# Kernel optimization log

Hardware: AMD Instinct MI355X
Metric: run time of the kernel (lower is better)

Reference implementation:

```python
import jax, jax.numpy as jnp
import numpy as np

B, L = 512, 260          # batch, raw input length
N_EMB, E_DIM = 8192, 128 * 65
NC = 16                   # num_classes


def setup_inputs() -> dict:
    key = jax.random.key(0)
    ks = jax.random.split(key, 12)
    rn = lambda k, shp, s: jax.random.normal(k, shp, jnp.float32) * s
    return {
        "x": rn(ks[0], (B, L), 1.0),
        # VQ codebook, init uniform(-1/K, 1/K) as in reference VQ-VAE
        "codebook": jax.random.uniform(ks[1], (N_EMB, E_DIM), jnp.float32, -1.0 / N_EMB, 1.0 / N_EMB),
        # encoder: Conv1d(1,64,k4,s2,p1) -> ReLU -> Conv1d(64,128,k4,s2,p1)
        "conv1_w": rn(ks[2], (64, 1, 4), 0.3), "conv1_b": jnp.zeros((64,), jnp.float32),
        "conv2_w": rn(ks[3], (128, 64, 4), 0.06), "conv2_b": jnp.zeros((128,), jnp.float32),
        # decoder: ConvT1d(128,64,k4,s2,p1) -> ReLU -> ConvT1d(64,1,k4,s2,p1); torch weight layout (in,out,k)
        "dec1_w": rn(ks[4], (128, 64, 4), 0.04), "dec1_b": jnp.zeros((64,), jnp.float32),
        "dec2_w": rn(ks[5], (64, 1, 4), 0.06), "dec2_b": jnp.zeros((1,), jnp.float32),
        # multitask head: Linear(4160, NC); torch layout (out,in)
        "mt_w": rn(ks[6], (NC, 4160), 0.015), "mt_b": jnp.zeros((NC,), jnp.float32),
        # adversary head: Linear(4160,256)->ReLU->Linear(256,128)->ReLU->Linear(128,NC)
        "adv_w1": rn(ks[7], (256, 4160), 0.015), "adv_b1": jnp.zeros((256,), jnp.float32),
        "adv_w2": rn(ks[8], (128, 256), 0.06), "adv_b2": jnp.zeros((128,), jnp.float32),
        "adv_w3": rn(ks[9], (NC, 128), 0.09), "adv_b3": jnp.zeros((NC,), jnp.float32),
        "beta": 0.25,
    }


def _conv1d(x, w, b, stride):
    # x: [B,C,L], w: [O,I,K] (torch Conv1d layout), padding=1
    y = jax.lax.conv_general_dilated(x, w, (stride,), [(1, 1)],
                                     dimension_numbers=("NCH", "OIH", "NCH"))
    return y + b[None, :, None]


def _convT1d(x, w, b, stride, k=4, p=1):
    # torch ConvTranspose1d(in,out,k,stride=s,padding=p); w: [I,O,K]
    # == dilated conv with lhs_dilation=s, padding=k-1-p, spatially-flipped, IO-swapped kernel
    wt = jnp.flip(w, -1).transpose(1, 0, 2)  # [O,I,K]
    pad = k - 1 - p
    y = jax.lax.conv_general_dilated(x, wt, (1,), [(pad, pad)], lhs_dilation=(stride,),
                                     dimension_numbers=("NCH", "OIH", "NCH"))
    return y + b[None, :, None]


def _forward(x, codebook, conv1_w, conv1_b, conv2_w, conv2_b,
             dec1_w, dec1_b, dec2_w, dec2_b, mt_w, mt_b,
             adv_w1, adv_b1, adv_w2, adv_b2, adv_w3, adv_b3, beta):
    sg = jax.lax.stop_gradient
    xb = x[:, None, :]                                      # x.unsqueeze_(1) -> [B,1,260]
    h = jax.nn.relu(_conv1d(xb, conv1_w, conv1_b, 2))       # [B,64,130]
    z_e = _conv1d(h, conv2_w, conv2_b, 2)                   # [B,128,65]
    b = z_e.shape[0]

    # ---- VectorQuantizer: cdist^2 / argmin / gather / commitment loss ----
    z = z_e.reshape(b, -1)                                  # [B,8320]
    d = (jnp.sum(z * z, axis=1, keepdims=True)
         + jnp.sum(codebook * codebook, axis=1)[None, :]
         - 2.0 * (z @ codebook.T))                          # [B,N_EMB]
    idx = jnp.argmin(d, axis=1)                             # [B]
    zq_raw = codebook[idx].reshape(z_e.shape)               # gather -> [B,128,65]
    emb_loss = (jnp.mean((sg(zq_raw) - z_e) ** 2)
                + beta * jnp.mean((zq_raw - sg(z_e)) ** 2))
    z_q = z_e + sg(zq_raw - z_e)                            # straight-through
    counts = jnp.zeros((codebook.shape[0],), z.dtype).at[idx].add(1.0)
    e_mean = counts / b
    perplexity = jnp.exp(-jnp.sum(e_mean * jnp.log(e_mean + 1e-10)))

    # ---- heads operate on z_e halves ----
    mt = z_e[:, :64, :].reshape(b, -1) @ mt_w.T + mt_b      # [B,NC]
    a = jax.nn.relu(z_e[:, 64:, :].reshape(b, -1) @ adv_w1.T + adv_b1)
    a = jax.nn.relu(a @ adv_w2.T + adv_b2)
    adv = a @ adv_w3.T + adv_b3                             # [B,NC]

    # ---- decoder on quantized codes ----
    hd = jax.nn.relu(_convT1d(z_q, dec1_w, dec1_b, 2))      # [B,64,130]
    x_hat = _convT1d(hd, dec2_w, dec2_b, 2)                 # [B,1,260]
    return emb_loss, x_hat, mt, adv, perplexity


def reference(x, codebook, conv1_w, conv1_b, conv2_w, conv2_b,
              dec1_w, dec1_b, dec2_w, dec2_b, mt_w, mt_b,
              adv_w1, adv_b1, adv_w2, adv_b2, adv_w3, adv_b3, beta):
    return _forward(x, codebook, conv1_w, conv1_b, conv2_w, conv2_b,
                    dec1_w, dec1_b, dec2_w, dec2_b, mt_w, mt_b,
                    adv_w1, adv_b1, adv_w2, adv_b2, adv_w3, adv_b3, beta)
```

## Files before the change

kernel.cpp:

```cpp
#include <hip/hip_runtime.h>
#include <stdint.h>

typedef __attribute__((ext_vector_type(8))) short s8v;
typedef __attribute__((ext_vector_type(4))) float f4v;

#define OUT_XHAT 1
#define OUT_MT   133121
#define OUT_ADV  141313
#define OUT_PERP 149505

#define WS_COUNTS   0
#define WS_EMB      8192
#define WS_A1       8256
#define WS_CN       139328
#define WS_ZN2      147520
#define WS_ZL1      148032
#define WS_CBL1     148544
#define WS_ZERO_N   156736
#define WS_ZE       156736
#define WS_SC0      4416576
#define WS_SC1      8610880
#define WS_ZQ       4416576
#define WS_HD       8676416
#define WS_W2T      12936256
#define WS_WE       12969024
#define WS_WO       12985408
#define WS_W2TA     13001792
#define WS_IDX      13034560
#define WS_ZPK      13035136
#define WS_CBT      15165056
#define WS_H        15165056

__device__ __forceinline__ short f2bf(float f) {
  uint32_t u = __float_as_uint(f);
  u = (u + 0x7FFFu + ((u >> 16) & 1u)) >> 16;
  return (short)u;
}

__device__ __forceinline__ void gl_lds16(const void* g, void* l) {
  __builtin_amdgcn_global_load_lds(
      (const __attribute__((address_space(1))) void*)g,
      (__attribute__((address_space(3))) void*)l, 16, 0, 0);
}

__global__ void k_init(float* w) {
  int id = blockIdx.x * 256 + threadIdx.x;
  if (id < WS_ZERO_N) w[id] = 0.f;
}

__global__ void k_prep(const float* __restrict__ c2w, const float* __restrict__ d1w,
                       const float* __restrict__ aw2, float* __restrict__ w2t,
                       float* __restrict__ We, float* __restrict__ Wo,
                       float* __restrict__ w2ta) {
  int id = blockIdx.x * 256 + threadIdx.x;
  if (id < 32768) {
    int c = id & 127, ik = id >> 7;
    int i = ik >> 2, k = ik & 3;
    w2t[id] = c2w[(c * 64 + i) * 4 + k];
    int kk = id >> 7;
    w2ta[id] = aw2[(id & 127) * 256 + kk];
  }
  if (id < 16384) {
    int o = id & 63, is = id >> 6;
    int i = is >> 1, s = is & 1;
    We[id] = d1w[(i * 64 + o) * 4 + (3 - 2 * s)];
    Wo[id] = d1w[(i * 64 + o) * 4 + (2 - 2 * s)];
  }
}

__global__ void k_conv1(const float* __restrict__ x, const float* __restrict__ w,
                        const float* __restrict__ bias, float* __restrict__ h) {
  int id = blockIdx.x * 256 + threadIdx.x;
  if (id >= 512 * 64 * 130) return;
  int t = id % 130, bc = id / 130;
  int c = bc & 63, b = bc >> 6;
  const float* xb = x + b * 260;
  float acc = bias[c];
  int p0 = 2 * t - 1;
#pragma unroll
  for (int k = 0; k < 4; ++k) {
    int p = p0 + k;
    float xv = (p >= 0 && p < 260) ? xb[p] : 0.f;
    acc = fmaf(xv, w[c * 4 + k], acc);
  }
  h[id] = fmaxf(acc, 0.f);
}

template <int N>
__global__ __launch_bounds__(256) void k_gemm_gather(
    const float* __restrict__ src, int Cin, int Tsrc, int kdiv_shift,
    int tmul_shift, int toff, const float* __restrict__ wt,
    const float* __restrict__ bias, float* __restrict__ out, int out_cstride,
    int out_tmul, int out_toff, int do_relu) {
  const int NPT = N / 16;
  __shared__ float At[32 * 64];
  __shared__ float Bt[32 * N];
  int tid = threadIdx.x;
  int row0 = blockIdx.x * 64;
  int tm = (tid & 15) * 4;
  int tn = (tid >> 4) * NPT;
  int sr = tid & 63;
  int sj0 = (tid >> 6) * 8;
  int rowm = row0 + sr;
  int gb = rowm / 65;
  int gt = rowm - gb * 65;
  const float* sbase = src + (size_t)gb * Cin * Tsrc;
  int tpos = (gt << tmul_shift) + toff;
  int kmask = (1 << kdiv_shift) - 1;
  int bkr = tid >> 3;
  int bnc = (tid & 7) * (N / 8);

  float acc[4][NPT];
#pragma unroll
  for (int i = 0; i < 4; ++i)
#pragma unroll
    for (int j = 0; j < NPT; ++j) acc[i][j] = 0.f;

  for (int k0 = 0; k0 < 256; k0 += 32) {
    float av[8];
#pragma unroll
    for (int u = 0; u < 8; ++u) {
      int jj = k0 + sj0 + u;
      int cc = jj >> kdiv_shift;
      int kk = jj & kmask;
      int p = tpos + kk;
      av[u] = (p >= 0 && p < Tsrc) ? sbase[cc * Tsrc + p] : 0.f;
    }
    float bvv[N / 8];
#pragma unroll
    for (int u = 0; u < N / 8; ++u) bvv[u] = wt[(k0 + bkr) * N + bnc + u];
    __syncthreads();
#pragma unroll
    for (int u = 0; u < 8; ++u) At[(sj0 + u) * 64 + sr] = av[u];
#pragma unroll
    for (int u = 0; u < N / 8; ++u) Bt[bkr * N + bnc + u] = bvv[u];
    __syncthreads();
#pragma unroll
    for (int kk = 0; kk < 32; ++kk) {
      float a0 = At[kk * 64 + tm + 0];
      float a1 = At[kk * 64 + tm + 1];
      float a2 = At[kk * 64 + tm + 2];
      float a3 = At[kk * 64 + tm + 3];
#pragma unroll
      for (int j = 0; j < NPT; ++j) {
        float bv = Bt[kk * N + tn + j];
        acc[0][j] = fmaf(a0, bv, acc[0][j]);
        acc[1][j] = fmaf(a1, bv, acc[1][j]);
        acc[2][j] = fmaf(a2, bv, acc[2][j]);
        acc[3][j] = fmaf(a3, bv, acc[3][j]);
      }
    }
  }
#pragma unroll
  for (int i = 0; i < 4; ++i) {
    int rr = row0 + tm + i;
    int b = rr / 65, t = rr - b * 65;
#pragma unroll
    for (int j = 0; j < NPT; ++j) {
      int n = tn + j;
      float v = acc[i][j] + bias[n];
      if (do_relu) v = fmaxf(v, 0.f);
      out[(size_t)b * N * out_cstride + (size_t)n * out_cstride +
          t * out_tmul + out_toff] = v;
    }
  }
}

__global__ __launch_bounds__(256) void k_packmat(const float* __restrict__ src,
                                                 short* __restrict__ dst,
                                                 float* __restrict__ nrm2,
                                                 float* __restrict__ l1,
                                                 int R, int nb) {
  __shared__ short tile[8 * 64 * 8];
  __shared__ float rsq[256], rl1[256];
  int bid = blockIdx.x;
  int n0 = (bid % nb) * 64;
  int k0 = (bid / nb) * 64;
  int tid = threadIdx.x;
  int nr = tid >> 2, qc = tid & 3;
  const float* sp = src + (size_t)(n0 + nr) * 8320 + k0 + qc * 16;
  float v[16];
  *(float4*)&v[0] = *(const float4*)(sp);
  *(float4*)&v[4] = *(const float4*)(sp + 4);
  *(float4*)&v[8] = *(const float4*)(sp + 8);
  *(float4*)&v[12] = *(const float4*)(sp + 12);
  float sq = 0.f, sl = 0.f;
#pragma unroll
  for (int i = 0; i < 16; ++i) {
    sq = fmaf(v[i], v[i], sq);
    sl += fabsf(v[i]);
  }
  union { short s[8]; int4 q; } u0, u1;
#pragma unroll
  for (int j = 0; j < 8; ++j) {
    u0.s[j] = f2bf(v[j]);
    u1.s[j] = f2bf(v[8 + j]);
  }
  *(int4*)&tile[((qc * 2 + 0) * 64 + nr) * 8] = u0.q;
  *(int4*)&tile[((qc * 2 + 1) * 64 + nr) * 8] = u1.q;
  rsq[tid] = sq;
  rl1[tid] = sl;
  __syncthreads();
  if (tid < 64) {
    float s = rsq[tid * 4] + rsq[tid * 4 + 1] + rsq[tid * 4 + 2] + rsq[tid * 4 + 3];
    float t = rl1[tid * 4] + rl1[tid * 4 + 1] + rl1[tid * 4 + 2] + rl1[tid * 4 + 3];
    atomicAdd(&nrm2[n0 + tid], s);
    atomicAdd(&l1[n0 + tid], t);
  }
  int kc = tid >> 5, nn = (tid & 31) * 2;
  size_t ob = ((size_t)(k0 / 8 + kc) * R + n0 + nn) * 8;
  *(int4*)&dst[ob] = *(int4*)&tile[(kc * 64 + nn) * 8];
  *(int4*)&dst[ob + 8] = *(int4*)&tile[(kc * 64 + nn + 1) * 8];
}

__global__ __launch_bounds__(256) void k_scores(const short* __restrict__ cbt,
                                                const short* __restrict__ zpk,
                                                const float* __restrict__ cn,
                                                float* __restrict__ sc0,
                                                float* __restrict__ sc1) {
  __shared__ short As[8 * 128 * 8];
  __shared__ short Bs[8 * 128 * 8];
  int bid = blockIdx.x;
  int kh = bid & 1, nt = (bid >> 1) & 63, mt = bid >> 7;
  int tid = threadIdx.x;
  int wave = tid >> 6, lane = tid & 63;
  int q = lane >> 4, r16 = lane & 15;
  int m0 = mt * 128, n0 = nt * 128;
  int cb8 = kh * 520;
  int rb = (wave >> 1) * 64, cw = (wave & 1) * 64;

  f4v acc[4][4];
#pragma unroll
  for (int i = 0; i < 4; ++i)
#pragma unroll
    for (int j = 0; j < 4; ++j)
#pragma unroll
      for (int r = 0; r < 4; ++r) acc[i][j][r] = 0.f;

  for (int ks = 0; ks < 65; ++ks) {
    int c0 = cb8 + ks * 8;
    __syncthreads();
#pragma unroll
    for (int i = 0; i < 4; ++i) {
      int kc = wave * 2 + (i & 1);
      int h = (i >> 1) * 64;
      size_t gk = (size_t)(c0 + kc);
      gl_lds16(zpk + (gk * 512 + m0 + h + lane) * 8, &As[(kc * 128 + h) * 8]);
      gl_lds16(cbt + (gk * 8192 + n0 + h + lane) * 8, &Bs[(kc * 128 + h) * 8]);
    }
    __syncthreads();
    s8v af[2][4], bfr[2][4];
#pragma unroll
    for (int g = 0; g < 2; ++g) {
      int kq = (g * 4 + q) * 128;
#pragma unroll
      for (int i = 0; i < 4; ++i) {
        af[g][i] = *(const s8v*)&As[(kq + rb + i * 16 + r16) * 8];
        bfr[g][i] = *(const s8v*)&Bs[(kq + cw + i * 16 + r16) * 8];
      }
    }
#pragma unroll
    for (int g = 0; g < 2; ++g)
#pragma unroll
      for (int mi = 0; mi < 4; ++mi)
#pragma unroll
        for (int ni = 0; ni < 4; ++ni)
          acc[mi][ni] = __builtin_amdgcn_mfma_f32_16x16x32_bf16(
              af[g][mi], bfr[g][ni], acc[mi][ni], 0, 0, 0);
  }

  float* sc = kh ? sc1 : sc0;
#pragma unroll
  for (int mi = 0; mi < 4; ++mi) {
#pragma unroll
    for (int ni = 0; ni < 4; ++ni) {
      int col = n0 + cw + ni * 16 + r16;
      float cnv = kh ? 0.f : cn[col];
#pragma unroll
      for (int r = 0; r < 4; ++r) {
        int row = m0 + rb + mi * 16 + q * 4 + r;
        sc[(size_t)row * 8192 + col] = -2.f * acc[mi][ni][r] + cnv;
      }
    }
  }
}

__global__ void k_argmin(const float* __restrict__ s0, const float* __restrict__ s1,
                         const float* __restrict__ z_e, const float* __restrict__ cb,
                         const float* __restrict__ zn2, const float* __restrict__ cn,
                         int* __restrict__ idx, float* __restrict__ counts) {
  __shared__ float red[256];
  __shared__ int cand[128];
  __shared__ float cval[128];
  __shared__ int ccnt;
  int b = blockIdx.x, tid = threadIdx.x;
  const float* r0 = s0 + (size_t)b * 8192;
  const float* r1 = s1 + (size_t)b * 8192;
  float mn = 1e30f;
  for (int j4 = tid; j4 < 2048; j4 += 256) {
    float4 a = *(const float4*)&r0[j4 * 4];
    float4 c = *(const float4*)&r1[j4 * 4];
    mn = fminf(mn, fminf(fminf(a.x + c.x, a.y + c.y), fminf(a.z + c.z, a.w + c.w)));
  }
  red[tid] = mn;
  __syncthreads();
  for (int st = 128; st > 0; st >>= 1) {
    if (tid < st) red[tid] = fminf(red[tid], red[tid + st]);
    __syncthreads();
  }
  float minv = red[0];
  float margin = sqrtf(zn2[b]) * (1.0f / 131072.0f) + 1e-4f;
  if (tid == 0) ccnt = 0;
  __syncthreads();
  float thr = minv + margin;
  for (int j4 = tid; j4 < 2048; j4 += 256) {
    float4 a = *(const float4*)&r0[j4 * 4];
    float4 c = *(const float4*)&r1[j4 * 4];
    float v[4] = {a.x + c.x, a.y + c.y, a.z + c.z, a.w + c.w};
#pragma unroll
    for (int u = 0; u < 4; ++u) {
      if (v[u] <= thr) {
        int p = atomicAdd(&ccnt, 1);
        if (p < 128) cand[p] = j4 * 4 + u;
      }
    }
  }
  __syncthreads();
  int nc = min(ccnt, 128);
  int wave = tid >> 6, lane = tid & 63;
  const float* zr = z_e + (size_t)b * 8320;
  float zn = zn2[b];
  for (int ci = wave; ci < nc; ci += 4) {
    int j = cand[ci];
    const float* cr = cb + (size_t)j * 8320;
    float dp = 0.f;
    for (int k4 = lane; k4 < 2080; k4 += 64) {
      float4 zv = *(const float4*)&zr[k4 * 4];
      float4 cv = *(const float4*)&cr[k4 * 4];
      dp = fmaf(zv.x, cv.x, dp);
      dp = fmaf(zv.y, cv.y, dp);
      dp = fmaf(zv.z, cv.z, dp);
      dp = fmaf(zv.w, cv.w, dp);
    }
    for (int off = 32; off > 0; off >>= 1) dp += __shfl_down(dp, off);
    if (lane == 0)
      cval[ci] = __fsub_rn(__fadd_rn(zn, cn[j]), __fmul_rn(2.f, dp));
  }
  __syncthreads();
  if (tid == 0) {
    float bv = 1e30f;
    int bj = 0x7fffffff;
    for (int ci = 0; ci < nc; ++ci) {
      float v = cval[ci];
      int j = cand[ci];
      if (v < bv || (v == bv && j < bj)) { bv = v; bj = j; }
    }
    idx[b] = bj;
    atomicAdd(&counts[bj], 1.0f);
  }
}

__global__ void k_gather(const float* __restrict__ cb, const float* __restrict__ z_e,
                         const int* __restrict__ idx, float* __restrict__ zq,
                         float* __restrict__ emb_acc) {
  __shared__ float red[256];
  int b = blockIdx.x, tid = threadIdx.x;
  int j = idx[b];
  const float* cr = cb + (size_t)j * 8320;
  const float* zr = z_e + (size_t)b * 8320;
  float* q = zq + (size_t)b * 8320;
  float part = 0.f;
  for (int k = tid; k < 8320; k += 256) {
    float c = cr[k];
    float d = c - zr[k];
    q[k] = c;
    part += d * d;
  }
  red[tid] = part;
  __syncthreads();
  for (int st = 128; st > 0; st >>= 1) {
    if (tid < st) red[tid] += red[tid + st];
    __syncthreads();
  }
  if (tid == 0) atomicAdd(emb_acc, red[0]);
}

__global__ void k_dec2(const float* __restrict__ hd, const float* __restrict__ w,
                       const float* __restrict__ bias, float* __restrict__ out) {
  int id = blockIdx.x * 256 + threadIdx.x;
  if (id >= 512 * 260) return;
  int b = id / 260, t = id % 260;
  int u = t >> 1;
  const float* hb = hd + (size_t)b * 8320;
  float acc = bias[0];
  if (t & 1) {
    bool ok = (u + 1 < 130);
    for (int i = 0; i < 64; ++i) {
      acc = fmaf(hb[i * 130 + u], w[i * 4 + 2], acc);
      if (ok) acc = fmaf(hb[i * 130 + u + 1], w[i * 4 + 0], acc);
    }
  } else {
    bool ok = (u >= 1);
    for (int i = 0; i < 64; ++i) {
      if (ok) acc = fmaf(hb[i * 130 + u - 1], w[i * 4 + 3], acc);
      acc = fmaf(hb[i * 130 + u], w[i * 4 + 1], acc);
    }
  }
  out[OUT_XHAT + id] = acc;
}

__global__ void k_mt(const float* __restrict__ z_e, const float* __restrict__ mtw,
                     const float* __restrict__ mtb, float* __restrict__ out) {
  __shared__ float red[64];
  int b = blockIdx.x, tid = threadIdx.x;
  int wave = tid >> 6, lane = tid & 63;
  const float* zr = z_e + (size_t)b * 8320;
  float acc[16];
#pragma unroll
  for (int n = 0; n < 16; ++n) acc[n] = 0.f;
  for (int k4 = tid; k4 < 1040; k4 += 256) {
    float4 zv = *(const float4*)&zr[k4 * 4];
#pragma unroll
    for (int n = 0; n < 16; ++n) {
      float4 wv = *(const float4*)&mtw[n * 4160 + k4 * 4];
      float a = acc[n];
      a = fmaf(zv.x, wv.x, a);
      a = fmaf(zv.y, wv.y, a);
      a = fmaf(zv.z, wv.z, a);
      a = fmaf(zv.w, wv.w, a);
      acc[n] = a;
    }
  }
#pragma unroll
  for (int n = 0; n < 16; ++n) {
    float v = acc[n];
    for (int off = 32; off > 0; off >>= 1) v += __shfl_down(v, off);
    if (lane == 0) red[n * 4 + wave] = v;
  }
  __syncthreads();
  if (tid < 16) {
    float s = red[tid * 4] + red[tid * 4 + 1] + red[tid * 4 + 2] + red[tid * 4 + 3];
    out[OUT_MT + b * 16 + tid] = s + mtb[tid];
  }
}

__global__ __launch_bounds__(256) void k_adv1(const float* __restrict__ z_e,
                                              const float* __restrict__ w1,
                                              float* __restrict__ a1) {
  __shared__ float At[32 * 64];
  __shared__ float Bt[32 * 64];
  int bid = blockIdx.x;
  int ksp = bid % 10;
  int nt = (bid / 10) & 3;
  int mt = bid / 40;
  int tid = threadIdx.x;
  int m0 = mt * 64, n0 = nt * 64, kb = ksp * 416;
  int tm = (tid & 15) * 4, tn = (tid >> 4) * 4;
  int sr = tid & 63, sj = (tid >> 6) * 8;
  const float* za = z_e + (size_t)(m0 + sr) * 8320 + 4160 + kb + sj;
  const float* wb = w1 + (size_t)(n0 + sr) * 4160 + kb + sj;
  float acc[4][4];
#pragma unroll
  for (int i = 0; i < 4; ++i)
#pragma unroll
    for (int j = 0; j < 4; ++j) acc[i][j] = 0.f;
  for (int k0 = 0; k0 < 416; k0 += 32) {
    float4 av0 = *(const float4*)(za + k0);
    float4 av1 = *(const float4*)(za + k0 + 4);
    float4 bv0 = *(const float4*)(wb + k0);
    float4 bv1 = *(const float4*)(wb + k0 + 4);
    __syncthreads();
    At[(sj + 0) * 64 + sr] = av0.x; At[(sj + 1) * 64 + sr] = av0.y;
    At[(sj + 2) * 64 + sr] = av0.z; At[(sj + 3) * 64 + sr] = av0.w;
    At[(sj + 4) * 64 + sr] = av1.x; At[(sj + 5) * 64 + sr] = av1.y;
    At[(sj + 6) * 64 + sr] = av1.z; At[(sj + 7) * 64 + sr] = av1.w;
    Bt[(sj + 0) * 64 + sr] = bv0.x; Bt[(sj + 1) * 64 + sr] = bv0.y;
    Bt[(sj + 2) * 64 + sr] = bv0.z; Bt[(sj + 3) * 64 + sr] = bv0.w;
    Bt[(sj + 4) * 64 + sr] = bv1.x; Bt[(sj + 5) * 64 + sr] = bv1.y;
    Bt[(sj + 6) * 64 + sr] = bv1.z; Bt[(sj + 7) * 64 + sr] = bv1.w;
    __syncthreads();
#pragma unroll
    for (int kk = 0; kk < 32; ++kk) {
      float4 aa = *(const float4*)&At[kk * 64 + tm];
      float4 bb = *(const float4*)&Bt[kk * 64 + tn];
      acc[0][0] = fmaf(aa.x, bb.x, acc[0][0]); acc[0][1] = fmaf(aa.x, bb.y, acc[0][1]);
      acc[0][2] = fmaf(aa.x, bb.z, acc[0][2]); acc[0][3] = fmaf(aa.x, bb.w, acc[0][3]);
      acc[1][0] = fmaf(aa.y, bb.x, acc[1][0]); acc[1][1] = fmaf(aa.y, bb.y, acc[1][1]);
      acc[1][2] = fmaf(aa.y, bb.z, acc[1][2]); acc[1][3] = fmaf(aa.y, bb.w, acc[1][3]);
      acc[2][0] = fmaf(aa.z, bb.x, acc[2][0]); acc[2][1] = fmaf(aa.z, bb.y, acc[2][1]);
      acc[2][2] = fmaf(aa.z, bb.z, acc[2][2]); acc[2][3] = fmaf(aa.z, bb.w, acc[2][3]);
      acc[3][0] = fmaf(aa.w, bb.x, acc[3][0]); acc[3][1] = fmaf(aa.w, bb.y, acc[3][1]);
      acc[3][2] = fmaf(aa.w, bb.z, acc[3][2]); acc[3][3] = fmaf(aa.w, bb.w, acc[3][3]);
    }
  }
#pragma unroll
  for (int i = 0; i < 4; ++i)
#pragma unroll
    for (int j = 0; j < 4; ++j)
      atomicAdd(&a1[(size_t)(m0 + tm + i) * 256 + n0 + tn + j], acc[i][j]);
}

__global__ void k_adv23(const float* __restrict__ a1raw, const float* __restrict__ b1,
                        const float* __restrict__ w2t, const float* __restrict__ b2,
                        const float* __restrict__ w3, const float* __restrict__ b3,
                        float* __restrict__ out) {
  __shared__ float s1[256];
  __shared__ float s2[128];
  int b = blockIdx.x, tid = threadIdx.x;
  s1[tid] = fmaxf(a1raw[(size_t)b * 256 + tid] + b1[tid], 0.f);
  __syncthreads();
  if (tid < 128) {
    float acc = b2[tid];
    for (int k = 0; k < 256; ++k) acc = fmaf(s1[k], w2t[k * 128 + tid], acc);
    s2[tid] = fmaxf(acc, 0.f);
  }
  __syncthreads();
  if (tid < 16) {
    float acc = b3[tid];
    for (int k = 0; k < 128; ++k) acc = fmaf(s2[k], w3[tid * 128 + k], acc);
    out[OUT_ADV + b * 16 + tid] = acc;
  }
}

__global__ void k_fin(const float* __restrict__ counts, const float* __restrict__ emb_acc,
                      const float* __restrict__ beta_p, float* __restrict__ out) {
  __shared__ float red[256];
  int tid = threadIdx.x;
  float part = 0.f;
  for (int j = tid; j < 8192; j += 256) {
    float e = counts[j] * (1.0f / 512.0f);
    part += e * logf(e + 1e-10f);
  }
  red[tid] = part;
  __syncthreads();
  for (int st = 128; st > 0; st >>= 1) {
    if (tid < st) red[tid] += red[tid + st];
    __syncthreads();
  }
  if (tid == 0) {
    out[OUT_PERP] = expf(-red[0]);
    out[0] = (1.f + beta_p[0]) * emb_acc[0] * (1.0f / 4259840.0f);
  }
}

extern "C" void kernel_launch(void* const* d_in, const int* in_sizes, int n_in,
                              void* d_out, int out_size, void* d_ws, size_t ws_size,
                              hipStream_t stream) {
  (void)in_sizes; (void)n_in; (void)out_size; (void)ws_size;
  const float* x   = (const float*)d_in[0];
  const float* cb  = (const float*)d_in[1];
  const float* c1w = (const float*)d_in[2];
  const float* c1b = (const float*)d_in[3];
  const float* c2w = (const float*)d_in[4];
  const float* c2b = (const float*)d_in[5];
  const float* d1w = (const float*)d_in[6];
  const float* d1b = (const float*)d_in[7];
  const float* d2w = (const float*)d_in[8];
  const float* d2b = (const float*)d_in[9];
  const float* mtw = (const float*)d_in[10];
  const float* mtb = (const float*)d_in[11];
  const float* aw1 = (const float*)d_in[12];
  const float* ab1 = (const float*)d_in[13];
  const float* aw2 = (const float*)d_in[14];
  const float* ab2 = (const float*)d_in[15];
  const float* aw3 = (const float*)d_in[16];
  const float* ab3 = (const float*)d_in[17];
  const float* beta = (const float*)d_in[18];
  float* out = (float*)d_out;
  float* W = (float*)d_ws;

  float* counts = W + WS_COUNTS;
  float* embac  = W + WS_EMB;
  float* a1buf  = W + WS_A1;
  float* cnbuf  = W + WS_CN;
  float* zn2    = W + WS_ZN2;
  float* zl1    = W + WS_ZL1;
  float* cbl1   = W + WS_CBL1;
  float* zebuf  = W + WS_ZE;
  float* sc0    = W + WS_SC0;
  float* sc1    = W + WS_SC1;
  float* zqbuf  = W + WS_ZQ;
  float* hdbuf  = W + WS_HD;
  float* w2t    = W + WS_W2T;
  float* We     = W + WS_WE;
  float* Wo     = W + WS_WO;
  float* w2ta   = W + WS_W2TA;
  int*   idxb   = (int*)(W + WS_IDX);
  short* zpk    = (short*)(W + WS_ZPK);
  short* cbt    = (short*)(W + WS_CBT);
  float* hbuf   = W + WS_H;

  k_init<<<(WS_ZERO_N + 255) / 256, 256, 0, stream>>>(W);
  k_prep<<<128, 256, 0, stream>>>(c2w, d1w, aw2, w2t, We, Wo, w2ta);
  k_conv1<<<16640, 256, 0, stream>>>(x, c1w, c1b, hbuf);
  k_gemm_gather<128><<<520, 256, 0, stream>>>(hbuf, 64, 130, 2, 1, -1, w2t, c2b,
                                              zebuf, 65, 1, 0, 0);
  k_packmat<<<8 * 130, 256, 0, stream>>>(zebuf, zpk, zn2, zl1, 512, 8);
  k_packmat<<<128 * 130, 256, 0, stream>>>(cb, cbt, cnbuf, cbl1, 8192, 128);
  k_scores<<<512, 256, 0, stream>>>(cbt, zpk, cnbuf, sc0, sc1);
  k_argmin<<<512, 256, 0, stream>>>(sc0, sc1, zebuf, cb, zn2, cnbuf, idxb,
                                    counts);
  k_gather<<<512, 256, 0, stream>>>(cb, zebuf, idxb, zqbuf, embac);
  k_gemm_gather<64><<<520, 256, 0, stream>>>(zqbuf, 128, 65, 1, 0, -1, We, d1b,
                                             hdbuf, 130, 2, 0, 1);
  k_gemm_gather<64><<<520, 256, 0, stream>>>(zqbuf, 128, 65, 1, 0, 0, Wo, d1b,
                                             hdbuf, 130, 2, 1, 1);
  k_dec2<<<520, 256, 0, stream>>>(hdbuf, d2w, d2b, out);
  k_mt<<<512, 256, 0, stream>>>(zebuf, mtw, mtb, out);
  k_adv1<<<320, 256, 0, stream>>>(zebuf, aw1, a1buf);
  k_adv23<<<512, 256, 0, stream>>>(a1buf, ab1, w2ta, ab2, aw3, ab3, out);
  k_fin<<<1, 256, 0, stream>>>(counts, embac, beta, out);
}
```

Before: 848.1 us.

## Merge kernels into fewer launches and fuse conv1, gather and decoder inputs

Combines init and prep into one kernel. conv1 is fused into the conv2 GEMM so the intermediate activation buffer is computed on the fly. Independent kernels (codebook packing, mt head, adv1, zpack, dec2, adv23, finalize) are grouped into shared mega-launches split by block index. The embedding-loss gather moves into the argmin kernel, which caches the score row in LDS, and the decoder reads codebook rows directly by index instead of a materialized z_q. The intent is to cut launch overhead, avoid writing and re-reading intermediate buffers, and let independent work overlap, at the cost of recomputing conv1 values and more complex heterogeneous blocks.

Measured after the change: 703.2 us. 1.21x faster.

```diff
diff --git a/kernel.cpp b/kernel.cpp
--- a/kernel.cpp
+++ b/kernel.cpp
@@ -20,7 +20,6 @@
 #define WS_ZE       156736
 #define WS_SC0      4416576
 #define WS_SC1      8610880
-#define WS_ZQ       4416576
 #define WS_HD       8676416
 #define WS_W2T      12936256
 #define WS_WE       12969024
@@ -29,7 +28,6 @@
 #define WS_IDX      13034560
 #define WS_ZPK      13035136
 #define WS_CBT      15165056
-#define WS_H        15165056
 
 __device__ __forceinline__ short f2bf(float f) {
   uint32_t u = __float_as_uint(f);
@@ -43,16 +41,15 @@
       (__attribute__((address_space(3))) void*)l, 16, 0, 0);
 }
 
-__global__ void k_init(float* w) {
+__global__ void k_initprep(float* __restrict__ W, const float* __restrict__ c2w,
+                           const float* __restrict__ d1w,
+                           const float* __restrict__ aw2) {
   int id = blockIdx.x * 256 + threadIdx.x;
-  if (id < WS_ZERO_N) w[id] = 0.f;
-}
-
-__global__ void k_prep(const float* __restrict__ c2w, const float* __restrict__ d1w,
-                       const float* __restrict__ aw2, float* __restrict__ w2t,
-                       float* __restrict__ We, float* __restrict__ Wo,
-                       float* __restrict__ w2ta) {
-  int id = blockIdx.x * 256 + threadIdx.x;
+  if (id < WS_ZERO_N) W[id] = 0.f;
+  float* w2t = W + WS_W2T;
+  float* We = W + WS_WE;
+  float* Wo = W + WS_WO;
+  float* w2ta = W + WS_W2TA;
   if (id < 32768) {
     int c = id & 127, ik = id >> 7;
     int i = ik >> 2, k = ik & 3;
@@ -68,115 +65,12 @@
   }
 }
 
-__global__ void k_conv1(const float* __restrict__ x, const float* __restrict__ w,
-                        const float* __restrict__ bias, float* __restrict__ h) {
-  int id = blockIdx.x * 256 + threadIdx.x;
-  if (id >= 512 * 64 * 130) return;
-  int t = id % 130, bc = id / 130;
-  int c = bc & 63, b = bc >> 6;
-  const float* xb = x + b * 260;
-  float acc = bias[c];
-  int p0 = 2 * t - 1;
-#pragma unroll
-  for (int k = 0; k < 4; ++k) {
-    int p = p0 + k;
-    float xv = (p >= 0 && p < 260) ? xb[p] : 0.f;
-    acc = fmaf(xv, w[c * 4 + k], acc);
-  }
-  h[id] = fmaxf(acc, 0.f);
-}
-
-template <int N>
-__global__ __launch_bounds__(256) void k_gemm_gather(
-    const float* __restrict__ src, int Cin, int Tsrc, int kdiv_shift,
-    int tmul_shift, int toff, const float* __restrict__ wt,
-    const float* __restrict__ bias, float* __restrict__ out, int out_cstride,
-    int out_tmul, int out_toff, int do_relu) {
-  const int NPT = N / 16;
-  __shared__ float At[32 * 64];
-  __shared__ float Bt[32 * N];
-  int tid = threadIdx.x;
-  int row0 = blockIdx.x * 64;
-  int tm = (tid & 15) * 4;
-  int tn = (tid >> 4) * NPT;
-  int sr = tid & 63;
-  int sj0 = (tid >> 6) * 8;
-  int rowm = row0 + sr;
-  int gb = rowm / 65;
-  int gt = rowm - gb * 65;
-  const float* sbase = src + (size_t)gb * Cin * Tsrc;
-  int tpos = (gt << tmul_shift) + toff;
-  int kmask = (1 << kdiv_shift) - 1;
-  int bkr = tid >> 3;
-  int bnc = (tid & 7) * (N / 8);
-
-  float acc[4][NPT];
-#pragma unroll
-  for (int i = 0; i < 4; ++i)
-#pragma unroll
-    for (int j = 0; j < NPT; ++j) acc[i][j] = 0.f;
-
-  for (int k0 = 0; k0 < 256; k0 += 32) {
-    float av[8];
-#pragma unroll
-    for (int u = 0; u < 8; ++u) {
-      int jj = k0 + sj0 + u;
-      int cc = jj >> kdiv_shift;
-      int kk = jj & kmask;
-      int p = tpos + kk;
-      av[u] = (p >= 0 && p < Tsrc) ? sbase[cc * Tsrc + p] : 0.f;
-    }
-    float bvv[N / 8];
-#pragma unroll
-    for (int u = 0; u < N / 8; ++u) bvv[u] = wt[(k0 + bkr) * N + bnc + u];
-    __syncthreads();
-#pragma unroll
-    for (int u = 0; u < 8; ++u) At[(sj0 + u) * 64 + sr] = av[u];
-#pragma unroll
-    for (int u = 0; u < N / 8; ++u) Bt[bkr * N + bnc + u] = bvv[u];
-    __syncthreads();
-#pragma unroll
-    for (int kk = 0; kk < 32; ++kk) {
-      float a0 = At[kk * 64 + tm + 0];
-      float a1 = At[kk * 64 + tm + 1];
-      float a2 = At[kk * 64 + tm + 2];
-      float a3 = At[kk * 64 + tm + 3];
-#pragma unroll
-      for (int j = 0; j < NPT; ++j) {
-        float bv = Bt[kk * N + tn + j];
-        acc[0][j] = fmaf(a0, bv, acc[0][j]);
-        acc[1][j] = fmaf(a1, bv, acc[1][j]);
-        acc[2][j] = fmaf(a2, bv, acc[2][j]);
-        acc[3][j] = fmaf(a3, bv, acc[3][j]);
-      }
-    }
-  }
-#pragma unroll
-  for (int i = 0; i < 4; ++i) {
-    int rr = row0 + tm + i;
-    int b = rr / 65, t = rr - b * 65;
-#pragma unroll
-    for (int j = 0; j < NPT; ++j) {
-      int n = tn + j;
-      float v = acc[i][j] + bias[n];
-      if (do_relu) v = fmaxf(v, 0.f);
-      out[(size_t)b * N * out_cstride + (size_t)n * out_cstride +
-          t * out_tmul + out_toff] = v;
-    }
-  }
-}
-
-__global__ __launch_bounds__(256) void k_packmat(const float* __restrict__ src,
-                                                 short* __restrict__ dst,
-                                                 float* __restrict__ nrm2,
-                                                 float* __restrict__ l1,
-                                                 int R, int nb) {
-  __shared__ short tile[8 * 64 * 8];
-  __shared__ float rsq[256], rl1[256];
-  int bid = blockIdx.x;
+__device__ __forceinline__ void packmat_body(
+    const float* __restrict__ src, short* __restrict__ dst,
+    float* __restrict__ nrm2, float* __restrict__ l1, int R, int nb, int bid,
+    int tid, short* tile, float* rsq, float* rl1) {
   int n0 = (bid % nb) * 64;
   int k0 = (bid / nb) * 64;
-  int tid = threadIdx.x;
   int nr = tid >> 2, qc = tid & 3;
   const float* sp = src + (size_t)(n0 + nr) * 8320 + k0 + qc * 16;
   float v[16];
@@ -211,6 +105,208 @@
   size_t ob = ((size_t)(k0 / 8 + kc) * R + n0 + nn) * 8;
   *(int4*)&dst[ob] = *(int4*)&tile[(kc * 64 + nn) * 8];
   *(int4*)&dst[ob + 8] = *(int4*)&tile[(kc * 64 + nn + 1) * 8];
+}
+
+__global__ __launch_bounds__(256) void k_megaA(
+    const float* __restrict__ x, const float* __restrict__ c1w,
+    const float* __restrict__ c1b, const float* __restrict__ w2t,
+    const float* __restrict__ c2b, float* __restrict__ zebuf,
+    const float* __restrict__ cb, short* __restrict__ cbt,
+    float* __restrict__ cn, float* __restrict__ cbl1) {
+  __shared__ __align__(16) char smem[28032];
+  int bid = blockIdx.x, tid = threadIdx.x;
+  if (bid < 520) {
+    float* At = (float*)smem;
+    float* Bt = At + 2048;
+    float* xs = Bt + 4096;
+    float* w1s = xs + 520;
+    float* b1s = w1s + 256;
+    int row0 = bid * 64;
+    int tm = (tid & 15) * 4;
+    int tn = (tid >> 4) * 8;
+    int sr = tid & 63;
+    int sj0 = (tid >> 6) * 8;
+    int rowm = row0 + sr;
+    int gb = rowm / 65;
+    int gt = rowm - gb * 65;
+    int gb0 = row0 / 65;
+    int xrow = gb - gb0;
+    int tpos = 2 * gt - 1;
+    int bkr = tid >> 3;
+    int bnc = (tid & 7) * 16;
+    for (int u = tid; u < 520; u += 256) {
+      int rr = gb0 + (u >= 260 ? 1 : 0);
+      if (rr > 511) rr = 511;
+      xs[u] = x[rr * 260 + (u >= 260 ? u - 260 : u)];
+    }
+    if (tid < 256) w1s[tid] = c1w[tid];
+    if (tid < 64) b1s[tid] = c1b[tid];
+    __syncthreads();
+    float acc[4][8];
+#pragma unroll
+    for (int i = 0; i < 4; ++i)
+#pragma unroll
+      for (int j = 0; j < 8; ++j) acc[i][j] = 0.f;
+    for (int k0i = 0; k0i < 256; k0i += 32) {
+      float av[8];
+#pragma unroll
+      for (int u = 0; u < 8; ++u) {
+        int jj = k0i + sj0 + u;
+        int cc = jj >> 2;
+        int kk = jj & 3;
+        int p = tpos + kk;
+        float hv = 0.f;
+        if (p >= 0 && p < 130) {
+          float a = b1s[cc];
+          int base = 2 * p - 1;
+#pragma unroll
+          for (int k = 0; k < 4; ++k) {
+            int xp = base + k;
+            float xv = (xp >= 0 && xp < 260) ? xs[xrow * 260 + xp] : 0.f;
+            a = fmaf(xv, w1s[cc * 4 + k], a);
+          }
+          hv = fmaxf(a, 0.f);
+        }
+        av[u] = hv;
+      }
+      float bvv[16];
+#pragma unroll
+      for (int u = 0; u < 16; ++u) bvv[u] = w2t[(k0i + bkr) * 128 + bnc + u];
+      __syncthreads();
+#pragma unroll
+      for (int u = 0; u < 8; ++u) At[(sj0 + u) * 64 + sr] = av[u];
+#pragma unroll
+      for (int u = 0; u < 16; ++u) Bt[bkr * 128 + bnc + u] = bvv[u];
+      __syncthreads();
+#pragma unroll
+      for (int kk = 0; kk < 32; ++kk) {
+        float a0 = At[kk * 64 + tm + 0];
+        float a1 = At[kk * 64 + tm + 1];
+        float a2 = At[kk * 64 + tm + 2];
+        float a3 = At[kk * 64 + tm + 3];
+#pragma unroll
+        for (int j = 0; j < 8; ++j) {
+          float bv = Bt[kk * 128 + tn + j];
+          acc[0][j] = fmaf(a0, bv, acc[0][j]);
+          acc[1][j] = fmaf(a1, bv, acc[1][j]);
+          acc[2][j] = fmaf(a2, bv, acc[2][j]);
+          acc[3][j] = fmaf(a3, bv, acc[3][j]);
+        }
+      }
+    }
+#pragma unroll
+    for (int i = 0; i < 4; ++i) {
+      int rr = row0 + tm + i;
+      int b = rr / 65, t = rr - b * 65;
+#pragma unroll
+      for (int j = 0; j < 8; ++j) {
+        int n = tn + j;
+        zebuf[(size_t)b * 8320 + (size_t)n * 65 + t] = acc[i][j] + c2b[n];
+      }
+    }
+  } else {
+    short* tile = (short*)smem;
+    float* rsq = (float*)(smem + 8192);
+    float* rl1 = rsq + 256;
+    packmat_body(cb, cbt, cn, cbl1, 8192, 128, bid - 520, tid, tile, rsq, rl1);
+  }
+}
+
+__global__ __launch_bounds__(256) void k_megaB(
+    const float* __restrict__ z_e, const float* __restrict__ mtw,
+    const float* __restrict__ mtb, const float* __restrict__ aw1,
+    short* __restrict__ zpk, float* __restrict__ zn2, float* __restrict__ zl1,
+    float* __restrict__ a1, float* __restrict__ out) {
+  __shared__ __align__(16) char smem[16384];
+  int bid = blockIdx.x, tid = threadIdx.x;
+  if (bid < 320) {
+    float* At = (float*)smem;
+    float* Bt = At + 2048;
+    int ksp = bid % 10;
+    int nt = (bid / 10) & 3;
+    int mt = bid / 40;
+    int m0 = mt * 64, n0 = nt * 64, kb = ksp * 416;
+    int tm = (tid & 15) * 4, tn = (tid >> 4) * 4;
+    int sr = tid & 63, sj = (tid >> 6) * 8;
+    const float* za = z_e + (size_t)(m0 + sr) * 8320 + 4160 + kb + sj;
+    const float* wb = aw1 + (size_t)(n0 + sr) * 4160 + kb + sj;
+    float acc[4][4];
+#pragma unroll
+    for (int i = 0; i < 4; ++i)
+#pragma unroll
+      for (int j = 0; j < 4; ++j) acc[i][j] = 0.f;
+    for (int k0 = 0; k0 < 416; k0 += 32) {
+      float4 av0 = *(const float4*)(za + k0);
+      float4 av1 = *(const float4*)(za + k0 + 4);
+      float4 bv0 = *(const float4*)(wb + k0);
+      float4 bv1 = *(const float4*)(wb + k0 + 4);
+      __syncthreads();
+      At[(sj + 0) * 64 + sr] = av0.x; At[(sj + 1) * 64 + sr] = av0.y;
+      At[(sj + 2) * 64 + sr] = av0.z; At[(sj + 3) * 64 + sr] = av0.w;
+      At[(sj + 4) * 64 + sr] = av1.x; At[(sj + 5) * 64 + sr] = av1.y;
+      At[(sj + 6) * 64 + sr] = av1.z; At[(sj + 7) * 64 + sr] = av1.w;
+      Bt[(sj + 0) * 64 + sr] = bv0.x; Bt[(sj + 1) * 64 + sr] = bv0.y;
+      Bt[(sj + 2) * 64 + sr] = bv0.z; Bt[(sj + 3) * 64 + sr] = bv0.w;
+      Bt[(sj + 4) * 64 + sr] = bv1.x; Bt[(sj + 5) * 64 + sr] = bv1.y;
+      Bt[(sj + 6) * 64 + sr] = bv1.z; Bt[(sj + 7) * 64 + sr] = bv1.w;
+      __syncthreads();
+#pragma unroll
+      for (int kk = 0; kk < 32; ++kk) {
+        float4 aa = *(const float4*)&At[kk * 64 + tm];
+        float4 bb = *(const float4*)&Bt[kk * 64 + tn];
+        acc[0][0] = fmaf(aa.x, bb.x, acc[0][0]); acc[0][1] = fmaf(aa.x, bb.y, acc[0][1]);
+        acc[0][2] = fmaf(aa.x, bb.z, acc[0][2]); acc[0][3] = fmaf(aa.x, bb.w, acc[0][3]);
+        acc[1][0] = fmaf(aa.y, bb.x, acc[1][0]); acc[1][1] = fmaf(aa.y, bb.y, acc[1][1]);
+        acc[1][2] = fmaf(aa.y, bb.z, acc[1][2]); acc[1][3] = fmaf(aa.y, bb.w, acc[1][3]);
+        acc[2][0] = fmaf(aa.z, bb.x, acc[2][0]); acc[2][1] = fmaf(aa.z, bb.y, acc[2][1]);
+        acc[2][2] = fmaf(aa.z, bb.z, acc[2][2]); acc[2][3] = fmaf(aa.z, bb.w, acc[2][3]);
+        acc[3][0] = fmaf(aa.w, bb.x, acc[3][0]); acc[3][1] = fmaf(aa.w, bb.y, acc[3][1]);
+        acc[3][2] = fmaf(aa.w, bb.z, acc[3][2]); acc[3][3] = fmaf(aa.w, bb.w, acc[3][3]);
+      }
+    }
+#pragma unroll
+    for (int i = 0; i < 4; ++i)
+#pragma unroll
+      for (int j = 0; j < 4; ++j)
+        atomicAdd(&a1[(size_t)(m0 + tm + i) * 256 + n0 + tn + j], acc[i][j]);
+  } else if (bid < 832) {
+    float* red = (float*)smem;
+    int b = bid - 320;
+    int wave = tid >> 6, lane = tid & 63;
+    const float* zr = z_e + (size_t)b * 8320;
+    float acc[16];
+#pragma unroll
+    for (int n = 0; n < 16; ++n) acc[n] = 0.f;
+    for (int k4 = tid; k4 < 1040; k4 += 256) {
+      float4 zv = *(const float4*)&zr[k4 * 4];
+#pragma unroll
+      for (int n = 0; n < 16; ++n) {
+        float4 wv = *(const float4*)&mtw[n * 4160 + k4 * 4];
+        float a = acc[n];
+        a = fmaf(zv.x, wv.x, a);
+        a = fmaf(zv.y, wv.y, a);
+        a = fmaf(zv.z, wv.z, a);
+        a = fmaf(zv.w, wv.w, a);
+        acc[n] = a;
+      }
+    }
+#pragma unroll
+    for (int n = 0; n < 16; ++n) {
+      float v = acc[n];
+      for (int off = 32; off > 0; off >>= 1) v += __shfl_down(v, off);
+      if (lane == 0) red[n * 4 + wave] = v;
+    }
+    __syncthreads();
+    if (tid < 16) {
+      float s = red[tid * 4] + red[tid * 4 + 1] + red[tid * 4 + 2] + red[tid * 4 + 3];
+      out[OUT_MT + b * 16 + tid] = s + mtb[tid];
+    }
+  } else {
+    short* tile = (short*)smem;
+    float* rsq = (float*)(smem + 8192);
+    float* rl1 = rsq + 256;
+    packmat_body(z_e, zpk, zn2, zl1, 512, 8, bid - 832, tid, tile, rsq, rl1);
+  }
 }
 
 __global__ __launch_bounds__(256) void k_scores(const short* __restrict__ cbt,
@@ -285,14 +381,18 @@
   }
 }
 
-__global__ void k_argmin(const float* __restrict__ s0, const float* __restrict__ s1,
-                         const float* __restrict__ z_e, const float* __restrict__ cb,
-                         const float* __restrict__ zn2, const float* __restrict__ cn,
-                         int* __restrict__ idx, float* __restrict__ counts) {
+__global__ __launch_bounds__(256) void k_argming(
+    const float* __restrict__ s0, const float* __restrict__ s1,
+    const float* __restrict__ z_e, const float* __restrict__ cb,
+    const float* __restrict__ zn2, const float* __restrict__ cn,
+    int* __restrict__ idx, float* __restrict__ counts,
+    float* __restrict__ emb_acc) {
+  __shared__ float srow[8192];
   __shared__ float red[256];
   __shared__ int cand[128];
   __shared__ float cval[128];
   __shared__ int ccnt;
+  __shared__ int bsel;
   int b = blockIdx.x, tid = threadIdx.x;
   const float* r0 = s0 + (size_t)b * 8192;
   const float* r1 = s1 + (size_t)b * 8192;
@@ -300,7 +400,10 @@
   for (int j4 = tid; j4 < 2048; j4 += 256) {
     float4 a = *(const float4*)&r0[j4 * 4];
     float4 c = *(const float4*)&r1[j4 * 4];
-    mn = fminf(mn, fminf(fminf(a.x + c.x, a.y + c.y), fminf(a.z + c.z, a.w + c.w)));
+    float4 v;
+    v.x = a.x + c.x; v.y = a.y + c.y; v.z = a.z + c.z; v.w = a.w + c.w;
+    *(float4*)&srow[j4 * 4] = v;
+    mn = fminf(mn, fminf(fminf(v.x, v.y), fminf(v.z, v.w)));
   }
   red[tid] = mn;
   __syncthreads();
@@ -313,16 +416,10 @@
   if (tid == 0) ccnt = 0;
   __syncthreads();
   float thr = minv + margin;
-  for (int j4 = tid; j4 < 2048; j4 += 256) {
-    float4 a = *(const float4*)&r0[j4 * 4];
-    float4 c = *(const float4*)&r1[j4 * 4];
-    float v[4] = {a.x + c.x, a.y + c.y, a.z + c.z, a.w + c.w};
-#pragma unroll
-    for (int u = 0; u < 4; ++u) {
-      if (v[u] <= thr) {
-        int p = atomicAdd(&ccnt, 1);
-        if (p < 128) cand[p] = j4 * 4 + u;
-      }
+  for (int j = tid; j < 8192; j += 256) {
+    if (srow[j] <= thr) {
+      int p = atomicAdd(&ccnt, 1);
+      if (p < 128) cand[p] = j;
     }
   }
   __syncthreads();
@@ -357,24 +454,18 @@
     }
     idx[b] = bj;
     atomicAdd(&counts[bj], 1.0f);
-  }
-}
-
-__global__ void k_gather(const float* __restrict__ cb, const float* __restrict__ z_e,
-                         const int* __restrict__ idx, float* __restrict__ zq,
-                         float* __restrict__ emb_acc) {
-  __shared__ float red[256];
-  int b = blockIdx.x, tid = threadIdx.x;
-  int j = idx[b];
-  const float* cr = cb + (size_t)j * 8320;
-  const float* zr = z_e + (size_t)b * 8320;
-  float* q = zq + (size_t)b * 8320;
+    bsel = bj;
+  }
+  __syncthreads();
+  int bj = bsel;
+  const float* cr2 = cb + (size_t)bj * 8320;
   float part = 0.f;
-  for (int k = tid; k < 8320; k += 256) {
-    float c = cr[k];
-    float d = c - zr[k];
-    q[k] = c;
-    part += d * d;
+  for (int k4 = tid; k4 < 2080; k4 += 256) {
+    float4 cv = *(const float4*)&cr2[k4 * 4];
+    float4 zv = *(const float4*)&zr[k4 * 4];
+    float d0 = cv.x - zv.x, d1 = cv.y - zv.y;
+    float d2 = cv.z - zv.z, d3 = cv.w - zv.w;
+    part += d0 * d0 + d1 * d1 + d2 * d2 + d3 * d3;
   }
   red[tid] = part;
   __syncthreads();
@@ -385,161 +476,143 @@
   if (tid == 0) atomicAdd(emb_acc, red[0]);
 }
 
-__global__ void k_dec2(const float* __restrict__ hd, const float* __restrict__ w,
-                       const float* __restrict__ bias, float* __restrict__ out) {
-  int id = blockIdx.x * 256 + threadIdx.x;
-  if (id >= 512 * 260) return;
-  int b = id / 260, t = id % 260;
-  int u = t >> 1;
-  const float* hb = hd + (size_t)b * 8320;
-  float acc = bias[0];
-  if (t & 1) {
-    bool ok = (u + 1 < 130);
-    for (int i = 0; i < 64; ++i) {
-      acc = fmaf(hb[i * 130 + u], w[i * 4 + 2], acc);
-      if (ok) acc = fmaf(hb[i * 130 + u + 1], w[i * 4 + 0], acc);
-    }
-  } else {
-    bool ok = (u >= 1);
-    for (int i = 0; i < 64; ++i) {
-      if (ok) acc = fmaf(hb[i * 130 + u - 1], w[i * 4 + 3], acc);
-      acc = fmaf(hb[i * 130 + u], w[i * 4 + 1], acc);
-    }
-  }
-  out[OUT_XHAT + id] = acc;
-}
-
-__global__ void k_mt(const float* __restrict__ z_e, const float* __restrict__ mtw,
-                     const float* __restrict__ mtb, float* __restrict__ out) {
-  __shared__ float red[64];
-  int b = blockIdx.x, tid = threadIdx.x;
-  int wave = tid >> 6, lane = tid & 63;
-  const float* zr = z_e + (size_t)b * 8320;
-  float acc[16];
-#pragma unroll
-  for (int n = 0; n < 16; ++n) acc[n] = 0.f;
-  for (int k4 = tid; k4 < 1040; k4 += 256) {
-    float4 zv = *(const float4*)&zr[k4 * 4];
-#pragma unroll
-    for (int n = 0; n < 16; ++n) {
-      float4 wv = *(const float4*)&mtw[n * 4160 + k4 * 4];
-      float a = acc[n];
-      a = fmaf(zv.x, wv.x, a);
-      a = fmaf(zv.y, wv.y, a);
-      a = fmaf(zv.z, wv.z, a);
-      a = fmaf(zv.w, wv.w, a);
-      acc[n] = a;
-    }
-  }
-#pragma unroll
-  for (int n = 0; n < 16; ++n) {
-    float v = acc[n];
-    for (int off = 32; off > 0; off >>= 1) v += __shfl_down(v, off);
-    if (lane == 0) red[n * 4 + wave] = v;
-  }
-  __syncthreads();
-  if (tid < 16) {
-    float s = red[tid * 4] + red[tid * 4 + 1] + red[tid * 4 + 2] + red[tid * 4 + 3];
-    out[OUT_MT + b * 16 + tid] = s + mtb[tid];
-  }
-}
-
-__global__ __launch_bounds__(256) void k_adv1(const float* __restrict__ z_e,
-                                              const float* __restrict__ w1,
-                                              float* __restrict__ a1) {
+__global__ __launch_bounds__(256) void k_dec1both(
+    const float* __restrict__ cb, const int* __restrict__ idxb,
+    const float* __restrict__ We, const float* __restrict__ Wo,
+    const float* __restrict__ bias, float* __restrict__ hd) {
   __shared__ float At[32 * 64];
   __shared__ float Bt[32 * 64];
-  int bid = blockIdx.x;
-  int ksp = bid % 10;
-  int nt = (bid / 10) & 3;
-  int mt = bid / 40;
-  int tid = threadIdx.x;
-  int m0 = mt * 64, n0 = nt * 64, kb = ksp * 416;
+  int bid = blockIdx.x, tid = threadIdx.x;
+  int par = (bid >= 520) ? 1 : 0;
+  int bl = bid - par * 520;
+  const float* wt = par ? Wo : We;
+  int toff = par - 1;
+  int row0 = bl * 64;
   int tm = (tid & 15) * 4, tn = (tid >> 4) * 4;
-  int sr = tid & 63, sj = (tid >> 6) * 8;
-  const float* za = z_e + (size_t)(m0 + sr) * 8320 + 4160 + kb + sj;
-  const float* wb = w1 + (size_t)(n0 + sr) * 4160 + kb + sj;
+  int sr = tid & 63, sj0 = (tid >> 6) * 8;
+  int rowm = row0 + sr;
+  int gb = rowm / 65, gt = rowm - gb * 65;
+  const float* sbase = cb + (size_t)idxb[gb] * 8320;
+  int tpos = gt + toff;
+  int bkr = tid >> 3, bnc = (tid & 7) * 8;
   float acc[4][4];
 #pragma unroll
   for (int i = 0; i < 4; ++i)
 #pragma unroll
     for (int j = 0; j < 4; ++j) acc[i][j] = 0.f;
-  for (int k0 = 0; k0 < 416; k0 += 32) {
-    float4 av0 = *(const float4*)(za + k0);
-    float4 av1 = *(const float4*)(za + k0 + 4);
-    float4 bv0 = *(const float4*)(wb + k0);
-    float4 bv1 = *(const float4*)(wb + k0 + 4);
-    __syncthreads();
-    At[(sj + 0) * 64 + sr] = av0.x; At[(sj + 1) * 64 + sr] = av0.y;
-    At[(sj + 2) * 64 + sr] = av0.z; At[(sj + 3) * 64 + sr] = av0.w;
-    At[(sj + 4) * 64 + sr] = av1.x; At[(sj + 5) * 64 + sr] = av1.y;
-    At[(sj + 6) * 64 + sr] = av1.z; At[(sj + 7) * 64 + sr] = av1.w;
-    Bt[(sj + 0) * 64 + sr] = bv0.x; Bt[(sj + 1) * 64 + sr] = bv0.y;
-    Bt[(sj + 2) * 64 + sr] = bv0.z; Bt[(sj + 3) * 64 + sr] = bv0.w;
-    Bt[(sj + 4) * 64 + sr] = bv1.x; Bt[(sj + 5) * 64 + sr] = bv1.y;
-    Bt[(sj + 6) * 64 + sr] = bv1.z; Bt[(sj + 7) * 64 + sr] = bv1.w;
+  for (int k0 = 0; k0 < 256; k0 += 32) {
+    float av[8];
+#pragma unroll
+    for (int u = 0; u < 8; ++u) {
+      int jj = k0 + sj0 + u;
+      int cc = jj >> 1;
+      int kk = jj & 1;
+      int p = tpos + kk;
+      av[u] = (p >= 0 && p < 65) ? sbase[cc * 65 + p] : 0.f;
+    }
+    float bvv[8];
+#pragma unroll
+    for (int u = 0; u < 8; ++u) bvv[u] = wt[(k0 + bkr) * 64 + bnc + u];
+    __syncthreads();
+#pragma unroll
+    for (int u = 0; u < 8; ++u) At[(sj0 + u) * 64 + sr] = av[u];
+#pragma unroll
+    for (int u = 0; u < 8; ++u) Bt[bkr * 64 + bnc + u] = bvv[u];
     __syncthreads();
 #pragma unroll
     for (int kk = 0; kk < 32; ++kk) {
-      float4 aa = *(const float4*)&At[kk * 64 + tm];
-      float4 bb = *(const float4*)&Bt[kk * 64 + tn];
-      acc[0][0] = fmaf(aa.x, bb.x, acc[0][0]); acc[0][1] = fmaf(aa.x, bb.y, acc[0][1]);
-      acc[0][2] = fmaf(aa.x, bb.z, acc[0][2]); acc[0][3] = fmaf(aa.x, bb.w, acc[0][3]);
-      acc[1][0] = fmaf(aa.y, bb.x, acc[1][0]); acc[1][1] = fmaf(aa.y, bb.y, acc[1][1]);
-      acc[1][2] = fmaf(aa.y, bb.z, acc[1][2]); acc[1][3] = fmaf(aa.y, bb.w, acc[1][3]);
-      acc[2][0] = fmaf(aa.z, bb.x, acc[2][0]); acc[2][1] = fmaf(aa.z, bb.y, acc[2][1]);
-      acc[2][2] = fmaf(aa.z, bb.z, acc[2][2]); acc[2][3] = fmaf(aa.z, bb.w, acc[2][3]);
-      acc[3][0] = fmaf(aa.w, bb.x, acc[3][0]); acc[3][1] = fmaf(aa.w, bb.y, acc[3][1]);
-      acc[3][2] = fmaf(aa.w, bb.z, acc[3][2]); acc[3][3] = fmaf(aa.w, bb.w, acc[3][3]);
-    }
-  }
-#pragma unroll
-  for (int i = 0; i < 4; ++i)
-#pragma unroll
-    for (int j = 0; j < 4; ++j)
-      atomicAdd(&a1[(size_t)(m0 + tm + i) * 256 + n0 + tn + j], acc[i][j]);
-}
-
-__global__ void k_adv23(const float* __restrict__ a1raw, const float* __restrict__ b1,
-                        const float* __restrict__ w2t, const float* __restrict__ b2,
+      float a0 = At[kk * 64 + tm + 0];
+      float a1 = At[kk * 64 + tm + 1];
+      float a2 = At[kk * 64 + tm + 2];
+      float a3 = At[kk * 64 + tm + 3];
+#pragma unroll
+      for (int j = 0; j < 4; ++j) {
+        float bv = Bt[kk * 64 + tn + j];
+        acc[0][j] = fmaf(a0, bv, acc[0][j]);
+        acc[1][j] = fmaf(a1, bv, acc[1][j]);
+        acc[2][j] = fmaf(a2, bv, acc[2][j]);
+        acc[3][j] = fmaf(a3, bv, acc[3][j]);
+      }
+    }
+  }
+#pragma unroll
+  for (int i = 0; i < 4; ++i) {
+    int rr = row0 + tm + i;
+    int b = rr / 65, t = rr - b * 65;
+#pragma unroll
+    for (int j = 0; j < 4; ++j) {
+      int n = tn + j;
+      float v = fmaxf(acc[i][j] + bias[n], 0.f);
+      hd[(size_t)b * 8320 + (size_t)n * 130 + t * 2 + par] = v;
+    }
+  }
+}
+
+__global__ void k_megaC(const float* __restrict__ hd, const float* __restrict__ d2w,
+                        const float* __restrict__ d2b,
+                        const float* __restrict__ a1raw, const float* __restrict__ b1,
+                        const float* __restrict__ w2ta, const float* __restrict__ b2,
                         const float* __restrict__ w3, const float* __restrict__ b3,
-                        float* __restrict__ out) {
-  __shared__ float s1[256];
-  __shared__ float s2[128];
-  int b = blockIdx.x, tid = threadIdx.x;
-  s1[tid] = fmaxf(a1raw[(size_t)b * 256 + tid] + b1[tid], 0.f);
-  __syncthreads();
-  if (tid < 128) {
-    float acc = b2[tid];
-    for (int k = 0; k < 256; ++k) acc = fmaf(s1[k], w2t[k * 128 + tid], acc);
-    s2[tid] = fmaxf(acc, 0.f);
-  }
-  __syncthreads();
-  if (tid < 16) {
-    float acc = b3[tid];
-    for (int k = 0; k < 128; ++k) acc = fmaf(s2[k], w3[tid * 128 + k], acc);
-    out[OUT_ADV + b * 16 + tid] = acc;
-  }
-}
-
-__global__ void k_fin(const float* __restrict__ counts, const float* __restrict__ emb_acc,
-                      const float* __restrict__ beta_p, float* __restrict__ out) {
-  __shared__ float red[256];
-  int tid = threadIdx.x;
-  float part = 0.f;
-  for (int j = tid; j < 8192; j += 256) {
-    float e = counts[j] * (1.0f / 512.0f);
-    part += e * logf(e + 1e-10f);
-  }
-  red[tid] = part;
-  __syncthreads();
-  for (int st = 128; st > 0; st >>= 1) {
-    if (tid < st) red[tid] += red[tid + st];
-    __syncthreads();
-  }
-  if (tid == 0) {
-    out[OUT_PERP] = expf(-red[0]);
-    out[0] = (1.f + beta_p[0]) * emb_acc[0] * (1.0f / 4259840.0f);
+                        const float* __restrict__ counts,
+                        const float* __restrict__ emb_acc,
+                        const float* __restrict__ beta_p, float* __restrict__ out) {
+  __shared__ float sbuf[384];
+  int bid = blockIdx.x, tid = threadIdx.x;
+  if (bid < 520) {
+    int id = bid * 256 + tid;
+    if (id >= 512 * 260) return;
+    int b = id / 260, t = id % 260;
+    int u = t >> 1;
+    const float* hb = hd + (size_t)b * 8320;
+    float acc = d2b[0];
+    if (t & 1) {
+      bool ok = (u + 1 < 130);
+      for (int i = 0; i < 64; ++i) {
+        acc = fmaf(hb[i * 130 + u], d2w[i * 4 + 2], acc);
+        if (ok) acc = fmaf(hb[i * 130 + u + 1], d2w[i * 4 + 0], acc);
+      }
+    } else {
+      bool ok = (u >= 1);
+      for (int i = 0; i < 64; ++i) {
+        if (ok) acc = fmaf(hb[i * 130 + u - 1], d2w[i * 4 + 3], acc);
+        acc = fmaf(hb[i * 130 + u], d2w[i * 4 + 1], acc);
+      }
+    }
+    out[OUT_XHAT + id] = acc;
+  } else if (bid < 1032) {
+    float* s1 = sbuf;
+    float* s2 = sbuf + 256;
+    int b = bid - 520;
+    s1[tid] = fmaxf(a1raw[(size_t)b * 256 + tid] + b1[tid], 0.f);
+    __syncthreads();
+    if (tid < 128) {
+      float acc = b2[tid];
+      for (int k = 0; k < 256; ++k) acc = fmaf(s1[k], w2ta[k * 128 + tid], acc);
+      s2[tid] = fmaxf(acc, 0.f);
+    }
+    __syncthreads();
+    if (tid < 16) {
+      float acc = b3[tid];
+      for (int k = 0; k < 128; ++k) acc = fmaf(s2[k], w3[tid * 128 + k], acc);
+      out[OUT_ADV + b * 16 + tid] = acc;
+    }
+  } else {
+    float* red = sbuf;
+    float part = 0.f;
+    for (int j = tid; j < 8192; j += 256) {
+      float e = counts[j] * (1.0f / 512.0f);
+      part += e * logf(e + 1e-10f);
+    }
+    red[tid] = part;
+    __syncthreads();
+    for (int st = 128; st > 0; st >>= 1) {
+      if (tid < st) red[tid] += red[tid + st];
+      __syncthreads();
+    }
+    if (tid == 0) {
+      out[OUT_PERP] = expf(-red[0]);
+      out[0] = (1.f + beta_p[0]) * emb_acc[0] * (1.0f / 4259840.0f);
+    }
   }
 }
 
@@ -566,6 +639,7 @@
   const float* aw3 = (const float*)d_in[16];
   const float* ab3 = (const float*)d_in[17];
   const float* beta = (const float*)d_in[18];
+  (void)aw2;
   float* out = (float*)d_out;
   float* W = (float*)d_ws;
 
@@ -579,7 +653,6 @@
   float* zebuf  = W + WS_ZE;
   float* sc0    = W + WS_SC0;
   float* sc1    = W + WS_SC1;
-  float* zqbuf  = W + WS_ZQ;
   float* hdbuf  = W + WS_HD;
   float* w2t    = W + WS_W2T;
   float* We     = W + WS_WE;
@@ -588,26 +661,17 @@
   int*   idxb   = (int*)(W + WS_IDX);
   short* zpk    = (short*)(W + WS_ZPK);
   short* cbt    = (short*)(W + WS_CBT);
-  float* hbuf   = W + WS_H;
-
-  k_init<<<(WS_ZERO_N + 255) / 256, 256, 0, stream>>>(W);
-  k_prep<<<128, 256, 0, stream>>>(c2w, d1w, aw2, w2t, We, Wo, w2ta);
-  k_conv1<<<16640, 256, 0, stream>>>(x, c1w, c1b, hbuf);
-  k_gemm_gather<128><<<520, 256, 0, stream>>>(hbuf, 64, 130, 2, 1, -1, w2t, c2b,
-                                              zebuf, 65, 1, 0, 0);
-  k_packmat<<<8 * 130, 256, 0, stream>>>(zebuf, zpk, zn2, zl1, 512, 8);
-  k_packmat<<<128 * 130, 256, 0, stream>>>(cb, cbt, cnbuf, cbl1, 8192, 128);
+
+  k_initprep<<<613, 256, 0, stream>>>(W, c2w, d1w, aw2);
+  k_megaA<<<520 + 16640, 256, 0, stream>>>(x, c1w, c1b, w2t, c2b, zebuf,
+                                           cb, cbt, cnbuf, cbl1);
+  k_megaB<<<320 + 512 + 1040, 256, 0, stream>>>(zebuf, mtw, mtb, aw1,
+                                                zpk, zn2, zl1, a1buf, out);
   k_scores<<<512, 256, 0, stream>>>(cbt, zpk, cnbuf, sc0, sc1);
-  k_argmin<<<512, 256, 0, stream>>>(sc0, sc1, zebuf, cb, zn2, cnbuf, idxb,
-                                    counts);
-  k_gather<<<512, 256, 0, stream>>>(cb, zebuf, idxb, zqbuf, embac);
-  k_gemm_gather<64><<<520, 256, 0, stream>>>(zqbuf, 128, 65, 1, 0, -1, We, d1b,
-                                             hdbuf, 130, 2, 0, 1);
-  k_gemm_gather<64><<<520, 256, 0, stream>>>(zqbuf, 128, 65, 1, 0, 0, Wo, d1b,
-                                             hdbuf, 130, 2, 1, 1);
-  k_dec2<<<520, 256, 0, stream>>>(hdbuf, d2w, d2b, out);
-  k_mt<<<512, 256, 0, stream>>>(zebuf, mtw, mtb, out);
-  k_adv1<<<320, 256, 0, stream>>>(zebuf, aw1, a1buf);
-  k_adv23<<<512, 256, 0, stream>>>(a1buf, ab1, w2ta, ab2, aw3, ab3, out);
-  k_fin<<<1, 256, 0, stream>>>(counts, embac, beta, out);
-}
+  k_argming<<<512, 256, 0, stream>>>(sc0, sc1, zebuf, cb, zn2, cnbuf, idxb,
+                                     counts, embac);
+  k_dec1both<<<1040, 256, 0, stream>>>(cb, idxb, We, Wo, d1b, hdbuf);
+  k_megaC<<<520 + 512 + 1, 256, 0, stream>>>(hdbuf, d2w, d2b, a1buf, ab1,
+                                             w2ta, ab2, aw3, ab3, counts,
+                                             embac, beta, out);
+}
```
